# Kernel optimization log

Hardware: AMD Instinct MI355X
Metric: run time of the kernel (lower is better)

Reference implementation:

```python
import jax, jax.numpy as jnp
import numpy as np


def setup_inputs() -> dict:
    key = jax.random.key(0)
    k1, k2 = jax.random.split(key)
    N, M, D = 8192, 8192, 512
    x = jax.random.normal(k1, (N, D), dtype=jnp.float32)
    y = jax.random.normal(k2, (M, D), dtype=jnp.float32)
    gamma = jnp.float32(1.0)
    return {"x": x, "y": y, "gamma": gamma}


def reference(x, y, gamma):
    # k(x, y) = exp(-gamma * ||x - y||^2)
    x = x.reshape(-1, x.shape[-1])
    y = y.reshape(-1, y.shape[-1])
    x_sq = jnp.sum(x * x, axis=-1)  # [N]
    y_sq = jnp.sum(y * y, axis=-1)  # [M]
    cross = x @ y.T                  # [N, M]
    sq_dist = x_sq[:, None] + y_sq[None, :] - 2.0 * cross
    sq_dist = jnp.maximum(sq_dist, 0.0)  # guard tiny negative roundoff
    return jnp.exp(-gamma * sq_dist)
```

## Files before the change

### kernel.cpp

```cpp
#include <hip/hip_runtime.h>
#include <hip/hip_bf16.h>

typedef unsigned short u16;
typedef __attribute__((ext_vector_type(8))) short bf16x8;
typedef __attribute__((ext_vector_type(4))) float f32x4;

typedef const __attribute__((address_space(1))) void gvoid_t;
typedef __attribute__((address_space(3))) void lvoid_t;

__device__ __forceinline__ void gload_lds16(const void* g, void* l) {
  __builtin_amdgcn_global_load_lds((gvoid_t*)g, (lvoid_t*)l, 16, 0, 0);
}

__device__ __forceinline__ u16 f2bf(float f) {
  union { float f; unsigned u; } a;
  a.f = f;
  unsigned r = (a.u + 0x7FFFu + ((a.u >> 16) & 1u)) >> 16;
  return (u16)r;
}

__global__ __launch_bounds__(128) void rbf_prep(
    const float* __restrict__ x, const float* __restrict__ y,
    u16* __restrict__ xb, u16* __restrict__ yb,
    float* __restrict__ xsq, float* __restrict__ ysq,
    int N, int M, int D) {
  int row = blockIdx.x;
  const float* src;
  u16* dst;
  float* sq;
  if (row < N) {
    src = x + (size_t)row * D;
    dst = xb + (size_t)row * D;
    sq = xsq + row;
  } else {
    int r = row - N;
    src = y + (size_t)r * D;
    dst = yb + (size_t)r * D;
    sq = ysq + r;
  }
  int t = threadIdx.x;
  float4 v = reinterpret_cast<const float4*>(src)[t];
  float s = v.x * v.x + v.y * v.y + v.z * v.z + v.w * v.w;
  ushort4 o;
  o.x = f2bf(v.x);
  o.y = f2bf(v.y);
  o.z = f2bf(v.z);
  o.w = f2bf(v.w);
  reinterpret_cast<ushort4*>(dst)[t] = o;
  #pragma unroll
  for (int off = 32; off > 0; off >>= 1) s += __shfl_down(s, off, 64);
  __shared__ float red[2];
  if ((t & 63) == 0) red[t >> 6] = s;
  __syncthreads();
  if (t == 0) sq[0] = red[0] + red[1];
}

#define BM 128
#define BN 128
#define BK 64

__global__ __launch_bounds__(256, 2) void rbf_gemm(
    const u16* __restrict__ xb, const u16* __restrict__ yb,
    const float* __restrict__ xsq, const float* __restrict__ ysq,
    const float* __restrict__ gptr, float* __restrict__ out,
    int N, int M, int D) {
  __shared__ u16 lds[2][2][BM * BK];

  int bid = blockIdx.x;
  int nbr = N / BM, nbc = M / BN;
  int trow, tcol;
  if (nbr == 64 && nbc == 64) {
    int xcd = bid & 7;
    int s = bid >> 3;
    int gr = s >> 6;
    int q = s & 63;
    trow = gr * 8 + (q & 7);
    tcol = xcd * 8 + (q >> 3);
  } else {
    int cpx = gridDim.x >> 3;
    int swz = (bid & 7) * cpx + (bid >> 3);
    trow = swz / nbc;
    tcol = swz % nbc;
  }
  int brow = trow * BM;
  int bcol = tcol * BN;

  int tid = threadIdx.x;
  int w = tid >> 6;
  int lane = tid & 63;
  int wm = w >> 1;
  int wn = w & 1;
  int fr = lane & 15;
  int fq = lane >> 4;

  int srow = lane >> 3;
  int scol = ((lane & 7) ^ srow) * 8;
  const u16* xsrc = xb + (size_t)(brow + w * 32 + srow) * D + scol;
  const u16* ysrc = yb + (size_t)(bcol + w * 32 + srow) * D + scol;
  int sdst = w * 2048;

  int cxor = (fr & 7) * 8;
  int colx0 = (fq * 8) ^ cxor;
  int colx1 = (32 + fq * 8) ^ cxor;
  int arow0 = (wm * 64 + fr) * 64;
  int brow0 = (wn * 64 + fr) * 64;

  f32x4 acc[4][4];
  #pragma unroll
  for (int m = 0; m < 4; ++m)
    #pragma unroll
    for (int n = 0; n < 4; ++n)
      acc[m][n] = (f32x4){0.f, 0.f, 0.f, 0.f};

  auto stage = [&](int kt, int b) {
    const u16* xs = xsrc + kt * 64;
    const u16* ys = ysrc + kt * 64;
    u16* la = &lds[b][0][sdst];
    u16* lb = &lds[b][1][sdst];
    #pragma unroll
    for (int i = 0; i < 4; ++i)
      gload_lds16(xs + (size_t)i * 8 * D, la + i * 512);
    #pragma unroll
    for (int i = 0; i < 4; ++i)
      gload_lds16(ys + (size_t)i * 8 * D, lb + i * 512);
  };

  int nkt = D >> 6;
  stage(0, 0);
  stage(1, 1);
  for (int t = 0; t < nkt; ++t) {
    int b = t & 1;
    if (t + 1 < nkt)
      asm volatile("s_waitcnt vmcnt(8)" ::: "memory");
    else
      asm volatile("s_waitcnt vmcnt(0)" ::: "memory");
    __builtin_amdgcn_sched_barrier(0);
    __builtin_amdgcn_s_barrier();
    __builtin_amdgcn_sched_barrier(0);

    const u16* A = &lds[b][0][0];
    const u16* B = &lds[b][1][0];
    bf16x8 af[4][2], bf[4][2];
    #pragma unroll
    for (int m = 0; m < 4; ++m) {
      af[m][0] = *(const bf16x8*)&A[arow0 + m * 1024 + colx0];
      af[m][1] = *(const bf16x8*)&A[arow0 + m * 1024 + colx1];
    }
    #pragma unroll
    for (int n = 0; n < 4; ++n) {
      bf[n][0] = *(const bf16x8*)&B[brow0 + n * 1024 + colx0];
      bf[n][1] = *(const bf16x8*)&B[brow0 + n * 1024 + colx1];
    }

    __builtin_amdgcn_s_setprio(1);
    #pragma unroll
    for (int m = 0; m < 4; ++m)
      #pragma unroll
      for (int n = 0; n < 4; ++n) {
        acc[m][n] = __builtin_amdgcn_mfma_f32_16x16x32_bf16(
            bf[n][0], af[m][0], acc[m][n], 0, 0, 0);
        acc[m][n] = __builtin_amdgcn_mfma_f32_16x16x32_bf16(
            bf[n][1], af[m][1], acc[m][n], 0, 0, 0);
      }
    __builtin_amdgcn_s_setprio(0);

    asm volatile("s_waitcnt lgkmcnt(0)" ::: "memory");
    __builtin_amdgcn_sched_barrier(0);
    __builtin_amdgcn_s_barrier();
    __builtin_amdgcn_sched_barrier(0);
    if (t + 2 < nkt) stage(t + 2, b);
  }

  float gl2 = gptr[0] * 1.44269504088896f;
  float m2gl2 = 2.0f * gl2;
  float4 gys[4];
  #pragma unroll
  for (int n = 0; n < 4; ++n) {
    float4 t4 = *reinterpret_cast<const float4*>(
        &ysq[bcol + wn * 64 + n * 16 + fq * 4]);
    gys[n].x = gl2 * t4.x;
    gys[n].y = gl2 * t4.y;
    gys[n].z = gl2 * t4.z;
    gys[n].w = gl2 * t4.w;
  }
  #pragma unroll
  for (int m = 0; m < 4; ++m) {
    int i = brow + wm * 64 + m * 16 + fr;
    float gxs = gl2 * xsq[i];
    size_t ro = (size_t)i * M;
    #pragma unroll
    for (int n = 0; n < 4; ++n) {
      int jb = bcol + wn * 64 + n * 16 + fq * 4;
      float4 e;
      e.x = exp2f(fminf(fmaf(m2gl2, acc[m][n][0], -(gxs + gys[n].x)), 0.f));
      e.y = exp2f(fminf(fmaf(m2gl2, acc[m][n][1], -(gxs + gys[n].y)), 0.f));
      e.z = exp2f(fminf(fmaf(m2gl2, acc[m][n][2], -(gxs + gys[n].z)), 0.f));
      e.w = exp2f(fminf(fmaf(m2gl2, acc[m][n][3], -(gxs + gys[n].w)), 0.f));
      *reinterpret_cast<float4*>(&out[ro + jb]) = e;
    }
  }
}

__global__ __launch_bounds__(256) void rbf_naive(
    const float* __restrict__ x, const float* __restrict__ y,
    const float* __restrict__ gptr, float* __restrict__ out,
    int N, int M, int D) {
  __shared__ float xs[16][17];
  __shared__ float ys[16][17];
  int nbn = M / 16;
  int brow = (blockIdx.x / nbn) * 16;
  int bcol = (blockIdx.x % nbn) * 16;
  int ti = threadIdx.x >> 4, tj = threadIdx.x & 15;
  float dacc = 0.f, xacc = 0.f, yacc = 0.f;
  for (int k0 = 0; k0 < D; k0 += 16) {
    xs[ti][tj] = x[(size_t)(brow + ti) * D + k0 + tj];
    ys[ti][tj] = y[(size_t)(bcol + ti) * D + k0 + tj];
    __syncthreads();
    #pragma unroll
    for (int kk = 0; kk < 16; ++kk) {
      float xv = xs[ti][kk], yv = ys[tj][kk];
      dacc += xv * yv;
      xacc += xv * xv;
      yacc += yv * yv;
    }
    __syncthreads();
  }
  float gamma = gptr[0];
  float d2 = fmaxf(xacc + yacc - 2.f * dacc, 0.f);
  out[(size_t)(brow + ti) * M + (bcol + tj)] = __expf(-gamma * d2);
}

extern "C" void kernel_launch(void* const* d_in, const int* in_sizes, int n_in,
                              void* d_out, int out_size, void* d_ws,
                              size_t ws_size, hipStream_t stream) {
  const float* x = (const float*)d_in[0];
  const float* y = (const float*)d_in[1];
  const float* g = (const float*)d_in[2];
  float* out = (float*)d_out;

  const int D = 512;
  const int N = in_sizes[0] / D;
  const int M = in_sizes[1] / D;

  size_t need = (size_t)(N + M) * D * sizeof(u16) + (size_t)(N + M) * sizeof(float);
  bool shapes_ok = (N % BM == 0) && (M % BN == 0) && (D % BK == 0) && (D / BK >= 2);

  if (ws_size >= need && shapes_ok) {
    u16* xb = (u16*)d_ws;
    u16* yb = xb + (size_t)N * D;
    float* xsq = (float*)(yb + (size_t)M * D);
    float* ysq = xsq + N;

    rbf_prep<<<N + M, 128, 0, stream>>>(x, y, xb, yb, xsq, ysq, N, M, D);
    int nwg = (N / BM) * (M / BN);
    rbf_gemm<<<nwg, 256, 0, stream>>>(xb, yb, xsq, ysq, g, out, N, M, D);
  } else {
    rbf_naive<<<(N / 16) * (M / 16), 256, 0, stream>>>(x, y, g, out, N, M, D);
  }
}
```

Baseline: 112.7 us.

## Process four column tiles per workgroup and overlap epilogue with next tile's loads

Each GEMM workgroup now walks four consecutive 128-wide column tiles in one flat K-pipeline instead of handling a single output tile. The exp/store epilogue for the previous tile runs after the next tile's first LDS fragments are read, so output writes overlap with prefetching and MFMA work. The grid shrinks fourfold and the XCD swizzle is remapped to column groups. In exchange, the stage indexing hardcodes 8 K-steps per tile (D=512), and fewer, longer workgroups may leave less room for tail balancing.

After: 117.3 us. 1.04x slower.

```diff
diff --git a/kernel.cpp b/kernel.cpp
--- a/kernel.cpp
+++ b/kernel.cpp
@@ -58,6 +58,7 @@
 #define BM 128
 #define BN 128
 #define BK 64
+#define NTILE 4
 
 __global__ __launch_bounds__(256, 2) void rbf_gemm(
     const u16* __restrict__ xb, const u16* __restrict__ yb,
@@ -67,23 +68,22 @@
   __shared__ u16 lds[2][2][BM * BK];
 
   int bid = blockIdx.x;
-  int nbr = N / BM, nbc = M / BN;
-  int trow, tcol;
-  if (nbr == 64 && nbc == 64) {
+  int nbr = N / BM;
+  int ncg = M / (BN * NTILE);
+  int trow, cg;
+  if (nbr == 64 && ncg == 16) {
     int xcd = bid & 7;
     int s = bid >> 3;
-    int gr = s >> 6;
-    int q = s & 63;
-    trow = gr * 8 + (q & 7);
-    tcol = xcd * 8 + (q >> 3);
+    trow = (s >> 4) * 8 + (s & 7);
+    cg = xcd * 2 + ((s >> 3) & 1);
   } else {
     int cpx = gridDim.x >> 3;
     int swz = (bid & 7) * cpx + (bid >> 3);
-    trow = swz / nbc;
-    tcol = swz % nbc;
+    trow = swz / ncg;
+    cg = swz % ncg;
   }
   int brow = trow * BM;
-  int bcol = tcol * BN;
+  int bcol0 = cg * (BN * NTILE);
 
   int tid = threadIdx.x;
   int w = tid >> 6;
@@ -96,7 +96,7 @@
   int srow = lane >> 3;
   int scol = ((lane & 7) ^ srow) * 8;
   const u16* xsrc = xb + (size_t)(brow + w * 32 + srow) * D + scol;
-  const u16* ysrc = yb + (size_t)(bcol + w * 32 + srow) * D + scol;
+  const u16* ysrc0 = yb + (size_t)(bcol0 + w * 32 + srow) * D + scol;
   int sdst = w * 2048;
 
   int cxor = (fr & 7) * 8;
@@ -105,6 +105,9 @@
   int arow0 = (wm * 64 + fr) * 64;
   int brow0 = (wn * 64 + fr) * 64;
 
+  float gl2 = gptr[0] * 1.44269504088896f;
+  float m2gl2 = 2.0f * gl2;
+
   f32x4 acc[4][4];
   #pragma unroll
   for (int m = 0; m < 4; ++m)
@@ -112,9 +115,12 @@
     for (int n = 0; n < 4; ++n)
       acc[m][n] = (f32x4){0.f, 0.f, 0.f, 0.f};
 
-  auto stage = [&](int kt, int b) {
+  auto stage = [&](int s) {
+    int kt = s & 7;
+    int bt = s >> 3;
+    int b = s & 1;
     const u16* xs = xsrc + kt * 64;
-    const u16* ys = ysrc + kt * 64;
+    const u16* ys = ysrc0 + (size_t)bt * BN * D + kt * 64;
     u16* la = &lds[b][0][sdst];
     u16* lb = &lds[b][1][sdst];
     #pragma unroll
@@ -125,12 +131,38 @@
       gload_lds16(ys + (size_t)i * 8 * D, lb + i * 512);
   };
 
-  int nkt = D >> 6;
-  stage(0, 0);
-  stage(1, 1);
-  for (int t = 0; t < nkt; ++t) {
-    int b = t & 1;
-    if (t + 1 < nkt)
+  auto epilogue = [&](int bt) {
+    int bcol = bcol0 + bt * BN;
+    #pragma unroll
+    for (int m = 0; m < 4; ++m) {
+      int i = brow + wm * 64 + m * 16 + fr;
+      float gxs = gl2 * xsq[i];
+      size_t ro = (size_t)i * M;
+      #pragma unroll
+      for (int n = 0; n < 4; ++n) {
+        int jb = bcol + wn * 64 + n * 16 + fq * 4;
+        float4 ys4 = *reinterpret_cast<const float4*>(&ysq[jb]);
+        float4 e;
+        e.x = exp2f(fminf(fmaf(m2gl2, acc[m][n][0], -fmaf(gl2, ys4.x, gxs)), 0.f));
+        e.y = exp2f(fminf(fmaf(m2gl2, acc[m][n][1], -fmaf(gl2, ys4.y, gxs)), 0.f));
+        e.z = exp2f(fminf(fmaf(m2gl2, acc[m][n][2], -fmaf(gl2, ys4.z, gxs)), 0.f));
+        e.w = exp2f(fminf(fmaf(m2gl2, acc[m][n][3], -fmaf(gl2, ys4.w, gxs)), 0.f));
+        *reinterpret_cast<float4*>(&out[ro + jb]) = e;
+      }
+    }
+    #pragma unroll
+    for (int m = 0; m < 4; ++m)
+      #pragma unroll
+      for (int n = 0; n < 4; ++n)
+        acc[m][n] = (f32x4){0.f, 0.f, 0.f, 0.f};
+  };
+
+  const int NS = (D >> 6) * NTILE;
+  stage(0);
+  stage(1);
+  for (int s = 0; s < NS; ++s) {
+    int b = s & 1;
+    if (s + 1 < NS)
       asm volatile("s_waitcnt vmcnt(8)" ::: "memory");
     else
       asm volatile("s_waitcnt vmcnt(0)" ::: "memory");
@@ -152,6 +184,10 @@
       bf[n][1] = *(const bf16x8*)&B[brow0 + n * 1024 + colx1];
     }
 
+    if (s >= 8 && (s & 7) == 0) epilogue((s >> 3) - 1);
+
+    asm volatile("s_waitcnt lgkmcnt(0)" ::: "memory");
+    __builtin_amdgcn_sched_barrier(0);
     __builtin_amdgcn_s_setprio(1);
     #pragma unroll
     for (int m = 0; m < 4; ++m)
@@ -164,41 +200,12 @@
       }
     __builtin_amdgcn_s_setprio(0);
 
-    asm volatile("s_waitcnt lgkmcnt(0)" ::: "memory");
     __builtin_amdgcn_sched_barrier(0);
     __builtin_amdgcn_s_barrier();
     __builtin_amdgcn_sched_barrier(0);
-    if (t + 2 < nkt) stage(t + 2, b);
-  }
-
-  float gl2 = gptr[0] * 1.44269504088896f;
-  float m2gl2 = 2.0f * gl2;
-  float4 gys[4];
-  #pragma unroll
-  for (int n = 0; n < 4; ++n) {
-    float4 t4 = *reinterpret_cast<const float4*>(
-        &ysq[bcol + wn * 64 + n * 16 + fq * 4]);
-    gys[n].x = gl2 * t4.x;
-    gys[n].y = gl2 * t4.y;
-    gys[n].z = gl2 * t4.z;
-    gys[n].w = gl2 * t4.w;
-  }
-  #pragma unroll
-  for (int m = 0; m < 4; ++m) {
-    int i = brow + wm * 64 + m * 16 + fr;
-    float gxs = gl2 * xsq[i];
-    size_t ro = (size_t)i * M;
-    #pragma unroll
-    for (int n = 0; n < 4; ++n) {
-      int jb = bcol + wn * 64 + n * 16 + fq * 4;
-      float4 e;
-      e.x = exp2f(fminf(fmaf(m2gl2, acc[m][n][0], -(gxs + gys[n].x)), 0.f));
-      e.y = exp2f(fminf(fmaf(m2gl2, acc[m][n][1], -(gxs + gys[n].y)), 0.f));
-      e.z = exp2f(fminf(fmaf(m2gl2, acc[m][n][2], -(gxs + gys[n].z)), 0.f));
-      e.w = exp2f(fminf(fmaf(m2gl2, acc[m][n][3], -(gxs + gys[n].w)), 0.f));
-      *reinterpret_cast<float4*>(&out[ro + jb]) = e;
-    }
-  }
+    if (s + 2 < NS) stage(s + 2);
+  }
+  epilogue(NTILE - 1);
 }
 
 __global__ __launch_bounds__(256) void rbf_naive(
@@ -243,7 +250,8 @@
   const int M = in_sizes[1] / D;
 
   size_t need = (size_t)(N + M) * D * sizeof(u16) + (size_t)(N + M) * sizeof(float);
-  bool shapes_ok = (N % BM == 0) && (M % BN == 0) && (D % BK == 0) && (D / BK >= 2);
+  bool shapes_ok = (N % BM == 0) && (M % (BN * NTILE) == 0) && (D % BK == 0) &&
+                   ((D / BK) >= 2);
 
   if (ws_size >= need && shapes_ok) {
     u16* xb = (u16*)d_ws;
@@ -252,7 +260,7 @@
     float* ysq = xsq + N;
 
     rbf_prep<<<N + M, 128, 0, stream>>>(x, y, xb, yb, xsq, ysq, N, M, D);
-    int nwg = (N / BM) * (M / BN);
+    int nwg = (N / BM) * (M / (BN * NTILE));
     rbf_gemm<<<nwg, 256, 0, stream>>>(xb, yb, xsq, ysq, g, out, N, M, D);
   } else {
     rbf_naive<<<(N / 16) * (M / 16), 256, 0, stream>>>(x, y, g, out, N, M, D);
```
